# Kernel optimization log

Measured on AMD Instinct MI355X. Metric: run time of the kernel, lower is better.

The kernel has to match this reference:

```python
import jax, jax.numpy as jnp
import numpy as np

T, B, N, C, H = 4, 4, 1024, 512, 8
D = C // H
EPS = 1e-5
TAU = 2.0
SCALE = 0.125


def _bn(x, g, b, m, v):
    # eval-mode BatchNorm1d over channel dim C (last axis here)
    return (x - m) * jax.lax.rsqrt(v + EPS) * g + b


def _lif(x, v_th=1.0):
    # multi-step LIF over leading T axis: v += (x - v)/tau; spike = H(v - vth);
    # hard reset to 0 (detach_reset); sigmoid surrogate (alpha=4) straight-through
    def step(v, xt):
        v = v + (xt - v) / TAU
        sg = jax.nn.sigmoid(4.0 * (v - v_th))
        hard = (v >= v_th).astype(x.dtype)
        spike = sg + jax.lax.stop_gradient(hard - sg)
        v = v * (1.0 - jax.lax.stop_gradient(spike))
        return v, spike
    _, s = jax.lax.scan(step, jnp.zeros_like(x[0]), x)
    return s


def _heads(y):
    # [T,B,N,C] -> [T,B,H,N,D]
    return y.reshape(T, B, N, H, D).transpose(0, 1, 3, 2, 4)


def _forward(x, s_x, q_w, q_b, q_g, q_bt, q_m, q_v,
             k_w, k_b, k_g, k_bt, k_m, k_v,
             v_w, v_b, v_g, v_bt, v_m, v_v,
             p_w, p_b, p_g, p_bt, p_m, p_v):
    # s_x is flattened but never used in the original forward
    q = _heads(_lif(_bn(x @ q_w.T + q_b, q_g, q_bt, q_m, q_v)))
    k = _heads(_lif(_bn(x @ k_w.T + k_b, k_g, k_bt, k_m, k_v)))
    v = _heads(_bn(x @ v_w.T + v_b, v_g, v_bt, v_m, v_v))  # no v_lif in original forward
    attn = jnp.einsum('tbhnd,tbhmd->tbhnm', q, k) * SCALE
    o = jnp.einsum('tbhnm,tbhmd->tbhnd', attn, v)
    o = o.transpose(0, 1, 3, 2, 4).reshape(T, B, N, C)
    return _bn(o @ p_w.T + p_b, p_g, p_bt, p_m, p_v)


def setup_inputs() -> dict:
    key = jax.random.key(0)
    ks = jax.random.split(key, 10)
    def w(k):
        return jax.random.normal(k, (C, C), jnp.float32) * 0.02
    ones = jnp.ones((C,), jnp.float32)
    zeros = jnp.zeros((C,), jnp.float32)
    return {
        'x': jax.random.normal(ks[0], (T, B, N, C), jnp.float32),
        's_x': jax.random.normal(ks[1], (T, B, N, C), jnp.float32),
        'q_w': w(ks[2]), 'q_b': zeros,
        'q_g': jax.random.uniform(ks[6], (C,), jnp.float32, 0.5, 1.5), 'q_bt': zeros, 'q_m': zeros, 'q_v': ones,
        'k_w': w(ks[3]), 'k_b': zeros,
        'k_g': jax.random.uniform(ks[7], (C,), jnp.float32, 0.5, 1.5), 'k_bt': zeros, 'k_m': zeros, 'k_v': ones,
        'v_w': w(ks[4]), 'v_b': zeros,
        'v_g': jax.random.uniform(ks[8], (C,), jnp.float32, 0.5, 1.5), 'v_bt': zeros, 'v_m': zeros, 'v_v': ones,
        'p_w': w(ks[5]), 'p_b': zeros,
        'p_g': jax.random.uniform(ks[9], (C,), jnp.float32, 0.5, 1.5), 'p_bt': zeros, 'p_m': zeros, 'p_v': ones,
    }


def reference(x, s_x, q_w, q_b, q_g, q_bt, q_m, q_v,
              k_w, k_b, k_g, k_bt, k_m, k_v,
              v_w, v_b, v_g, v_bt, v_m, v_v,
              p_w, p_b, p_g, p_bt, p_m, p_v):
    return _forward(x, s_x, q_w, q_b, q_g, q_bt, q_m, q_v,
                    k_w, k_b, k_g, k_bt, k_m, k_v,
                    v_w, v_b, v_g, v_bt, v_m, v_v,
                    p_w, p_b, p_g, p_bt, p_m, p_v)
```

## Files before the change

kernel.cpp:

```cpp
#include <hip/hip_runtime.h>


#define T_ 4
#define B_ 4
#define N_ 1024
#define C_ 512
#define H_ 8
#define M_ (T_*B_*N_)

typedef __bf16 bf16x8 __attribute__((ext_vector_type(8)));
typedef float  floatx4 __attribute__((ext_vector_type(4)));

__device__ __forceinline__ float bf2f(unsigned short u) {
  union { unsigned int i; float f; } v; v.i = ((unsigned int)u) << 16; return v.f;
}
__device__ __forceinline__ unsigned short f2bf(float f) {
  unsigned int x = __float_as_uint(f);
  return (unsigned short)((x + 0x7fffu + ((x >> 16) & 1u)) >> 16);
}

#define GLOAD16(gaddr, ldsbase) \
  __builtin_amdgcn_global_load_lds((__attribute__((address_space(1))) void*)(gaddr), \
                                   (__attribute__((address_space(3))) void*)(ldsbase), 16, 0, 0)

__global__ __launch_bounds__(256) void prep_split_x(const float* __restrict__ src,
                                                    unsigned short* __restrict__ dst,
                                                    int nelem) {
  const int idx = (blockIdx.x * 256 + threadIdx.x) * 4;
  if (idx >= nelem) return;
  const float4 v = *(const float4*)(src + idx);
  const int m = idx >> 9, k = idx & 511;
  const int t = m >> 12, b = (m >> 10) & 3, n = m & 1023;
  const int mp = (((b << 10) | n) << 2) | t;
  const size_t base = (size_t)mp * 1024 + k;
  float vv[4] = {v.x, v.y, v.z, v.w};
  unsigned short h[4], l[4];
#pragma unroll
  for (int j = 0; j < 4; ++j) { h[j] = f2bf(vv[j]); l[j] = f2bf(vv[j] - bf2f(h[j])); }
  *(ushort4*)(dst + base) = ushort4{h[0], h[1], h[2], h[3]};
  *(ushort4*)(dst + base + 512) = ushort4{l[0], l[1], l[2], l[3]};
}

__global__ __launch_bounds__(256) void prep_weights(const float* __restrict__ qw,
                                                    const float* __restrict__ kw,
                                                    const float* __restrict__ vw,
                                                    const float* __restrict__ pw,
                                                    unsigned short* __restrict__ Wqk3,
                                                    unsigned short* __restrict__ Wvb,
                                                    unsigned short* __restrict__ Wpb) {
  const int z = blockIdx.z;
  const int idx = (blockIdx.x * 256 + threadIdx.x) * 4;
  if (idx >= C_ * C_) return;
  const float* src = (z == 0) ? qw : (z == 1) ? kw : (z == 2) ? vw : pw;
  const float4 v = *(const float4*)(src + idx);
  if (z >= 2) {
    unsigned short* dst = (z == 2) ? Wvb : Wpb;
    *(ushort4*)(dst + idx) = ushort4{f2bf(v.x), f2bf(v.y), f2bf(v.z), f2bf(v.w)};
    return;
  }
  const int row = idx >> 9, k = idx & 511;
  unsigned short* dst = Wqk3 + (size_t)(z * 512) * 1536;
  const size_t base = (size_t)row * 1536 + k;
  float vv[4] = {v.x, v.y, v.z, v.w};
  unsigned short h[4], l[4];
#pragma unroll
  for (int j = 0; j < 4; ++j) { h[j] = f2bf(vv[j]); l[j] = f2bf(vv[j] - bf2f(h[j])); }
  ushort4 hi{h[0], h[1], h[2], h[3]};
  *(ushort4*)(dst + base) = hi;
  *(ushort4*)(dst + base + 512) = hi;
  *(ushort4*)(dst + base + 1024) = ushort4{l[0], l[1], l[2], l[3]};
}

struct BnParams { const float* p[20]; };
__global__ __launch_bounds__(256) void bn_prep(BnParams P, float* __restrict__ scl,
                                               float* __restrict__ sft) {
  const int o = blockIdx.x * 256 + threadIdx.x;
  const int grp = o >> 9, ci = o & 511;
  const float* bias = P.p[grp * 5 + 0];
  const float* g    = P.p[grp * 5 + 1];
  const float* bt   = P.p[grp * 5 + 2];
  const float* mu   = P.p[grp * 5 + 3];
  const float* var  = P.p[grp * 5 + 4];
  const float s = g[ci] * rsqrtf(var[ci] + 1e-5f);
  scl[o] = s;
  sft[o] = (bias[ci] - mu[ci]) * s + bt[ci];
}

struct Job2 {
  const unsigned short* A; int lda;
  const unsigned short* w; int ldb;
  int K, ldc, epi;
  const float* scl; const float* sft;
  float* out32; unsigned short* out16; unsigned short* out16b;
};

__global__ __launch_bounds__(512, 2) void gemm_bn(Job2 job, int lntile) {
  const int xcd = blockIdx.x & 7, slot = blockIdx.x >> 3;
  const int ntm1 = (1 << lntile) - 1;
  const int panel = xcd + 8 * (slot >> lntile);
  const int m0 = panel * 256;
  const int n0 = (slot & ntm1) * 256;

  const int tid = threadIdx.x;
  const int wv = tid >> 6, lane = tid & 63;
  const int wm = wv >> 1, wn = wv & 1;
  const int NT = job.K >> 5;

  __shared__ unsigned short AB[4][256 * 64];

  const int rloc = lane >> 3;
  const int ulog = (lane & 7) ^ rloc;
  const bool isA = ulog < 4;
  const unsigned short* bq[4];
#pragma unroll
  for (int q = 0; q < 4; ++q) {
    const int row = wv * 32 + q * 8 + rloc;
    bq[q] = isA ? job.A + (size_t)(m0 + row) * job.lda + ulog * 8
                : job.w + (size_t)(n0 + row) * job.ldb + (ulog - 4) * 8;
  }

#define ISSUE(T_, BUF_) do {                                                 \
    const int t_ = (T_);                                                     \
    const int off_ = isA ? ((t_ < 32 ? t_ : t_ - 32) << 5) : (t_ << 5);      \
    _Pragma("unroll")                                                        \
    for (int q = 0; q < 4; ++q)                                              \
      GLOAD16(bq[q] + off_, &AB[BUF_][(wv * 32 + q * 8) * 64]);              \
  } while (0)

  const int r15 = lane & 15;
  const int apos = (lane >> 4) ^ (lane & 7);
  const int bpos = (4 | (lane >> 4)) ^ (lane & 7);
  const int aoff = (wm * 64 + r15) * 64 + apos * 8;
  const int boff = (wn * 128 + r15) * 64 + bpos * 8;

  bf16x8 A0[4], A1[4], L0[4], L1[4], Hh[4];

#define RD_ALO(BUF_, AX, LX) do {                                            \
    const unsigned short* lb_ = &AB[BUF_][0];                                \
    _Pragma("unroll")                                                        \
    for (int i_ = 0; i_ < 4; ++i_) AX[i_] = *(const bf16x8*)(lb_ + aoff + i_ * 1024); \
    _Pragma("unroll")                                                        \
    for (int j_ = 0; j_ < 4; ++j_) LX[j_] = *(const bf16x8*)(lb_ + boff + j_ * 1024); \
  } while (0)

#define RD_HI(BUF_) do {                                                     \
    const unsigned short* lb_ = &AB[BUF_][0];                                \
    _Pragma("unroll")                                                        \
    for (int j_ = 0; j_ < 4; ++j_) Hh[j_] = *(const bf16x8*)(lb_ + boff + (4 + j_) * 1024); \
  } while (0)

#define MF_LO(AX, LX) do {                                                   \
    __builtin_amdgcn_s_setprio(1);                                           \
    _Pragma("unroll")                                                        \
    for (int i_ = 0; i_ < 4; ++i_)                                           \
    _Pragma("unroll")                                                        \
      for (int j_ = 0; j_ < 4; ++j_)                                         \
        acc[i_][j_] = __builtin_amdgcn_mfma_f32_16x16x32_bf16(AX[i_], LX[j_], acc[i_][j_], 0, 0, 0); \
    __builtin_amdgcn_s_setprio(0);                                           \
  } while (0)

#define MF_HI(AX) do {                                                       \
    __builtin_amdgcn_s_setprio(1);                                           \
    _Pragma("unroll")                                                        \
    for (int i_ = 0; i_ < 4; ++i_)                                           \
    _Pragma("unroll")                                                        \
      for (int j_ = 0; j_ < 4; ++j_)                                         \
        acc[i_][4 + j_] = __builtin_amdgcn_mfma_f32_16x16x32_bf16(AX[i_], Hh[j_], acc[i_][4 + j_], 0, 0, 0); \
    __builtin_amdgcn_s_setprio(0);                                           \
  } while (0)

#define MIDBAR(N_) do {                                                      \
    asm volatile("s_waitcnt vmcnt(" #N_ ")" ::: "memory");                   \
    __builtin_amdgcn_s_barrier();                                            \
    __builtin_amdgcn_sched_barrier(0);                                       \
  } while (0)

#define SLOT_I(KT_, BC_, BN_, AX, LX, AY, LY) do {                           \
    RD_HI(BC_); MF_LO(AX, LX);                                               \
    MIDBAR(4);                                                               \
    ISSUE((KT_) + 3, (BC_ + 3) & 3);                                         \
    RD_ALO(BN_, AY, LY); MF_HI(AX);                                          \
  } while (0)

  floatx4 acc[4][8];
#pragma unroll
  for (int i = 0; i < 4; ++i)
#pragma unroll
    for (int j = 0; j < 8; ++j) acc[i][j] = floatx4{0.f, 0.f, 0.f, 0.f};

  ISSUE(0, 0); ISSUE(1, 1); ISSUE(2, 2);
  asm volatile("s_waitcnt vmcnt(4)" ::: "memory");
  __builtin_amdgcn_s_barrier();
  __builtin_amdgcn_sched_barrier(0);
  RD_ALO(0, A0, L0);

  const int NG = (NT - 4) >> 2;
  for (int g = 0; g < NG; ++g) {
    const int g4 = g << 2;
    SLOT_I(g4 + 0, 0, 1, A0, L0, A1, L1);
    SLOT_I(g4 + 1, 1, 2, A1, L1, A0, L0);
    SLOT_I(g4 + 2, 2, 3, A0, L0, A1, L1);
    SLOT_I(g4 + 3, 3, 0, A1, L1, A0, L0);
  }
  SLOT_I(NT - 4, 0, 1, A0, L0, A1, L1);
  RD_HI(1); MF_LO(A1, L1); MIDBAR(4); RD_ALO(2, A0, L0); MF_HI(A1);
  RD_HI(2); MF_LO(A0, L0); MIDBAR(0); RD_ALO(3, A1, L1); MF_HI(A0);
  RD_HI(3); MF_LO(A1, L1); MF_HI(A1);

  float scl[8], sft[8];
#pragma unroll
  for (int j = 0; j < 8; ++j) {
    const int c = n0 + wn * 128 + j * 16 + r15;
    scl[j] = job.scl[c];
    sft[j] = job.sft[c];
  }
  const int rbase = m0 + wm * 64 + (lane >> 4) * 4;

  if (job.epi == 2 && n0 < 512) {
    const int cb = n0 + wn * 128 + r15;
#pragma unroll
    for (int i = 0; i < 4; ++i) {
      unsigned short spk[4][8];
#pragma unroll
      for (int j = 0; j < 8; ++j) {
        float vme = 0.f;
#pragma unroll
        for (int r = 0; r < 4; ++r) {
          const float y = acc[i][j][r] * scl[j] + sft[j];
          vme += (y - vme) * 0.5f;
          const bool sp = vme >= 1.0f;
          spk[r][j] = sp ? (unsigned short)0x3F80 : (unsigned short)0;
          if (sp) vme = 0.f;
        }
      }
#pragma unroll
      for (int r = 0; r < 4; ++r) {
        unsigned short* prow = job.out16 + (size_t)(rbase + 16 * i + r) * 512 + cb;
#pragma unroll
        for (int j = 0; j < 8; ++j) prow[j * 16] = spk[r][j];
      }
    }
  } else if (job.epi == 2) {
    __syncthreads();
    unsigned short* lds = &AB[0][0];
    const int gq = lane >> 4;
#pragma unroll
    for (int i = 0; i < 4; ++i) {
      const int n_loc = wm * 16 + 4 * i + gq;
#pragma unroll
      for (int j = 0; j < 8; ++j) {
        const int c_loc = wn * 128 + j * 16 + r15;
        const int colbase = c_loc * 64 + (n_loc ^ ((c_loc & 7) << 3));
        float vme = 0.f;
#pragma unroll
        for (int r = 0; r < 4; ++r) {
          const float y = acc[i][j][r] * scl[j] + sft[j];
          vme += (y - vme) * 0.5f;
          const bool sp = vme >= 1.0f;
          lds[r * 16384 + colbase] = sp ? (unsigned short)0x3F80 : (unsigned short)0;
          if (sp) vme = 0.f;
        }
      }
    }
    __syncthreads();
    const int b = panel >> 4, n0g = (panel & 15) * 64, cb = n0 - 512;
#pragma unroll
    for (int it = 0; it < 16; ++it) {
      const int rho = wv * 128 + it * 8 + (lane >> 3);
      const int t = rho >> 8, c = rho & 255;
      const int nb = lane & 7;
      const uint4 d = *(const uint4*)&lds[t * 16384 + c * 64 + ((nb ^ (c & 7)) << 3)];
      *(uint4*)(job.out16b + (size_t)((t * 4 + b) * 512 + cb + c) * 1024 + n0g + nb * 8) = d;
    }
  } else {
#pragma unroll
    for (int i = 0; i < 4; ++i)
#pragma unroll
      for (int r = 0; r < 4; ++r) {
        unsigned short* prow = job.out16 + (size_t)(rbase + 16 * i + r) * job.ldc + n0 + wn * 128 + r15;
#pragma unroll
        for (int j = 0; j < 8; ++j) prow[j * 16] = f2bf(acc[i][j][r] * scl[j] + sft[j]);
      }
  }
}

__global__ __launch_bounds__(512, 2) void gemm_bn128(Job2 job) {
  const int xcd = blockIdx.x & 7, slot = blockIdx.x >> 3;
  const int panel = xcd + 8 * (slot >> 1);
  const int m0 = panel * 128;
  const int n0 = (slot & 1) * 256;

  const int tid = threadIdx.x;
  const int wv = tid >> 6, lane = tid & 63;
  const int wm = wv >> 2, wn = wv & 3;

  __shared__ unsigned short ABS[4][384 * 32];

  const unsigned short* src[3];
#pragma unroll
  for (int g = 0; g < 3; ++g) {
    const int row = wv * 48 + g * 16 + (lane >> 2);
    const int ulog = (lane & 3) ^ (row & 3);
    src[g] = (row < 128) ? job.A + (size_t)(m0 + row) * job.lda + ulog * 8
                         : job.w + (size_t)(n0 + row - 128) * job.ldb + ulog * 8;
  }

#define ISSUE1(T_, BUF_) do {                                                \
    const int k0_ = (T_) << 5;                                               \
    _Pragma("unroll")                                                        \
    for (int g_ = 0; g_ < 3; ++g_)                                           \
      GLOAD16(src[g_] + k0_, &ABS[BUF_][(wv * 48 + g_ * 16) * 32]);          \
  } while (0)

  const int r15 = lane & 15;
  const int uoff = ((lane >> 4) ^ (r15 & 3)) << 3;
  const int arow0 = (wm * 64 + r15) * 32 + uoff;
  const int brow0 = (128 + wn * 64 + r15) * 32 + uoff;

  bf16x8 AX[4], BX[4], AY[4], BY[4];
#define RD1(BUF_, A_, B_) do {                                               \
    const unsigned short* lb_ = &ABS[BUF_][0];                               \
    _Pragma("unroll")                                                        \
    for (int i_ = 0; i_ < 4; ++i_) A_[i_] = *(const bf16x8*)(lb_ + arow0 + i_ * 512); \
    _Pragma("unroll")                                                        \
    for (int j_ = 0; j_ < 4; ++j_) B_[j_] = *(const bf16x8*)(lb_ + brow0 + j_ * 512); \
  } while (0)

#define MF1(A_, B_) do {                                                     \
    __builtin_amdgcn_s_setprio(1);                                           \
    _Pragma("unroll")                                                        \
    for (int i_ = 0; i_ < 4; ++i_)                                           \
    _Pragma("unroll")                                                        \
      for (int j_ = 0; j_ < 4; ++j_)                                         \
        acc[i_][j_] = __builtin_amdgcn_mfma_f32_16x16x32_bf16(A_[i_], B_[j_], acc[i_][j_], 0, 0, 0); \
    __builtin_amdgcn_s_setprio(0);                                           \
  } while (0)

#define MB1(N_) do {                                                         \
    asm volatile("s_waitcnt vmcnt(" #N_ ")" ::: "memory");                   \
    __builtin_amdgcn_s_barrier();                                            \
    __builtin_amdgcn_sched_barrier(0);                                       \
  } while (0)

  floatx4 acc[4][4];
#pragma unroll
  for (int i = 0; i < 4; ++i)
#pragma unroll
    for (int j = 0; j < 4; ++j) acc[i][j] = floatx4{0.f, 0.f, 0.f, 0.f};

  ISSUE1(0, 0); ISSUE1(1, 1); ISSUE1(2, 2);
  asm volatile("s_waitcnt vmcnt(6)" ::: "memory");
  __builtin_amdgcn_s_barrier();
  __builtin_amdgcn_sched_barrier(0);
  RD1(0, AX, BX);

#pragma unroll 1
  for (int kt = 0; kt < 12; kt += 2) {
    MB1(3); ISSUE1(kt + 3, (kt + 3) & 3); RD1((kt + 1) & 3, AY, BY); MF1(AX, BX);
    MB1(3); ISSUE1(kt + 4, (kt + 4) & 3); RD1((kt + 2) & 3, AX, BX); MF1(AY, BY);
  }
  MB1(3); ISSUE1(15, 3); RD1(1, AY, BY); MF1(AX, BX);
  MB1(3); RD1(2, AX, BX); MF1(AY, BY);
  MB1(0); RD1(3, AY, BY); MF1(AX, BX);
  MF1(AY, BY);

  float scl[4], sft[4];
#pragma unroll
  for (int j = 0; j < 4; ++j) {
    const int c = n0 + wn * 64 + j * 16 + r15;
    scl[j] = job.scl[c];
    sft[j] = job.sft[c];
  }
  const int rbase = m0 + wm * 64 + (lane >> 4) * 4;

  if (job.epi == 4) {
    __syncthreads();
    unsigned short* lds = &ABS[0][0];
    const int gq = lane >> 4;
#pragma unroll
    for (int i = 0; i < 4; ++i) {
      const int n_loc = wm * 16 + 4 * i + gq;
#pragma unroll
      for (int j = 0; j < 4; ++j) {
        const int c_loc = wn * 64 + j * 16 + r15;
        const int colbase = c_loc * 32 + (n_loc ^ (((c_loc >> 2) & 3) << 3));
#pragma unroll
        for (int r = 0; r < 4; ++r)
          lds[r * 8192 + colbase] = f2bf(acc[i][j][r] * scl[j] + sft[j]);
      }
    }
    __syncthreads();
    const int b = panel >> 5, n0g = (panel & 31) * 32;
#pragma unroll
    for (int it = 0; it < 8; ++it) {
      const int rho = wv * 128 + it * 16 + (lane >> 2);
      const int t = rho >> 8, c = rho & 255;
      const int nb = lane & 3;
      const uint4 d = *(const uint4*)&lds[t * 8192 + c * 32 + ((nb ^ ((c >> 2) & 3)) << 3)];
      *(uint4*)(job.out16b + (size_t)((t * 4 + b) * 512 + n0 + c) * 1024 + n0g + nb * 8) = d;
    }
  } else {
#pragma unroll
    for (int i = 0; i < 4; ++i)
#pragma unroll
      for (int r = 0; r < 4; ++r) {
        const int mp = rbase + 16 * i + r;
        const int t = mp & 3, bn = mp >> 2;
        const int mstd = (((t << 2) | (bn >> 10)) << 10) | (bn & 1023);
        float* prow = job.out32 + (size_t)mstd * 512 + n0 + wn * 64 + r15;
#pragma unroll
        for (int j = 0; j < 4; ++j) prow[j * 16] = acc[i][j][r] * scl[j] + sft[j];
      }
  }
}

__global__ __launch_bounds__(256) void kv_gemm(const unsigned short* __restrict__ ktr,
                                               const unsigned short* __restrict__ vtr,
                                               float* __restrict__ kvp) {
  const int bid = blockIdx.x;
  const int head = bid >> 1;
  const int mh = bid & 1;
  const int tb = head >> 3;
  const int h = head & 7;
  const int wv = threadIdx.x >> 6, lane = threadIdx.x & 63;
  const int m0 = mh * 512 + wv * 128;
  const size_t cbase = (size_t)tb * C_ + h * 64;
  const int rsel = lane & 15, koff = (lane >> 4) * 8;

  floatx4 acc[4][4];
#pragma unroll
  for (int i = 0; i < 4; ++i)
#pragma unroll
    for (int j = 0; j < 4; ++j) acc[i][j] = floatx4{0.f, 0.f, 0.f, 0.f};

#pragma unroll
  for (int s = 0; s < 4; ++s) {
    const int m = m0 + s * 32 + koff;
    bf16x8 a[4], b[4];
#pragma unroll
    for (int dt = 0; dt < 4; ++dt)
      a[dt] = *(const bf16x8*)(ktr + (cbase + dt * 16 + rsel) * N_ + m);
#pragma unroll
    for (int et = 0; et < 4; ++et)
      b[et] = *(const bf16x8*)(vtr + (cbase + et * 16 + rsel) * N_ + m);
#pragma unroll
    for (int dt = 0; dt < 4; ++dt)
#pragma unroll
      for (int et = 0; et < 4; ++et)
        acc[dt][et] = __builtin_amdgcn_mfma_f32_16x16x32_bf16(a[dt], b[et], acc[dt][et], 0, 0, 0);
  }

  float* outp = kvp + ((size_t)head * 8 + mh * 4 + wv) * 4096;
  const int dbase = (lane >> 4) * 4;
  const int e0 = lane & 15;
#pragma unroll
  for (int dt = 0; dt < 4; ++dt)
#pragma unroll
    for (int et = 0; et < 4; ++et)
#pragma unroll
      for (int r = 0; r < 4; ++r)
        outp[(dt * 16 + dbase + r) * 64 + et * 16 + e0] = acc[dt][et][r];
}

__global__ __launch_bounds__(256) void kv_reduce(const float* __restrict__ kvp,
                                                 unsigned short* __restrict__ kvt) {
  const int gid = blockIdx.x * 256 + threadIdx.x;
  const int idx4 = gid * 4;
  const int head = idx4 >> 12;
  const int rem = idx4 & 4095;
  const int e = rem >> 6, d0 = rem & 63;
  const float* p = kvp + (size_t)head * 8 * 4096;
  unsigned short rr[4];
#pragma unroll
  for (int j = 0; j < 4; ++j) {
    float s = 0.f;
#pragma unroll
    for (int pp = 0; pp < 8; ++pp) s += p[pp * 4096 + (d0 + j) * 64 + e];
    rr[j] = f2bf(0.125f * s);
  }
  uint2 o;
  o.x = (unsigned)rr[0] | ((unsigned)rr[1] << 16);
  o.y = (unsigned)rr[2] | ((unsigned)rr[3] << 16);
  *(uint2*)(kvt + idx4) = o;
}

__global__ __launch_bounds__(256) void av_gemm(const unsigned short* __restrict__ qs,
                                               const unsigned short* __restrict__ kvt,
                                               unsigned short* __restrict__ obuf) {
  const int bx = blockIdx.x;
  const int tb = bx >> 3, nt = bx & 7;
  const int t = tb >> 2, b = tb & 3;
  const int wv = threadIdx.x >> 6, lane = threadIdx.x & 63;
  const int n0 = nt * 128 + wv * 32;
  const int rsel = lane & 15, koff = (lane >> 4) * 8;

#pragma unroll 1
  for (int h = 0; h < H_; ++h) {
    floatx4 acc[2][4];
#pragma unroll
    for (int i = 0; i < 2; ++i)
#pragma unroll
      for (int j = 0; j < 4; ++j) acc[i][j] = floatx4{0.f, 0.f, 0.f, 0.f};
    const unsigned short* kvh = kvt + ((size_t)tb * 8 + h) * 4096;
#pragma unroll
    for (int s = 0; s < 2; ++s) {
      bf16x8 a[2], bv[4];
#pragma unroll
      for (int i = 0; i < 2; ++i) {
        const int n = n0 + i * 16 + rsel;
        a[i] = *(const bf16x8*)(qs + (size_t)((((b << 10) | n) << 2) | t) * 512 + h * 64 + s * 32 + koff);
      }
#pragma unroll
      for (int et = 0; et < 4; ++et)
        bv[et] = *(const bf16x8*)(kvh + (et * 16 + rsel) * 64 + s * 32 + koff);
#pragma unroll
      for (int i = 0; i < 2; ++i)
#pragma unroll
        for (int et = 0; et < 4; ++et)
          acc[i][et] = __builtin_amdgcn_mfma_f32_16x16x32_bf16(a[i], bv[et], acc[i][et], 0, 0, 0);
    }
#pragma unroll
    for (int i = 0; i < 2; ++i)
#pragma unroll
      for (int et = 0; et < 4; ++et)
#pragma unroll
        for (int r = 0; r < 4; ++r) {
          const int n = n0 + i * 16 + (lane >> 4) * 4 + r;
          obuf[(size_t)((((b << 10) | n) << 2) | t) * 512 + h * 64 + et * 16 + rsel] = f2bf(acc[i][et][r]);
        }
  }
}

extern "C" void kernel_launch(void* const* d_in, const int* in_sizes, int n_in,
                              void* d_out, int out_size, void* d_ws, size_t ws_size,
                              hipStream_t stream) {
  const float* x  = (const float*)d_in[0];
  const float* qw = (const float*)d_in[2];
  const float* kw = (const float*)d_in[8];
  const float* vw = (const float*)d_in[14];
  const float* pw = (const float*)d_in[20];

  char* ws = (char*)d_ws;
  unsigned short* X2   = (unsigned short*)(ws + 0);
  unsigned short* Wqk3 = (unsigned short*)(ws + 33554432ull);
  unsigned short* Wvb  = (unsigned short*)(ws + 36700160ull);
  unsigned short* Wpb  = (unsigned short*)(ws + 37224448ull);
  float*          scl  = (float*)(ws + 37748736ull);
  float*          sft  = (float*)(ws + 37756928ull);
  unsigned short* qsb  = (unsigned short*)(ws + 41943040ull);
  unsigned short* ktr  = (unsigned short*)(ws + 58720256ull);
  unsigned short* vtr  = (unsigned short*)(ws + 75497472ull);
  float*          kvp  = (float*)(ws + 92274688ull);
  unsigned short* kvt  = (unsigned short*)(ws + 109051904ull);
  unsigned short* ob   = (unsigned short*)(ws + 110100480ull);

  prep_split_x<<<dim3(M_ * C_ / 4 / 256), 256, 0, stream>>>(x, X2, M_ * C_);
  prep_weights<<<dim3(C_ * C_ / 4 / 256, 1, 4), 256, 0, stream>>>(qw, kw, vw, pw, Wqk3, Wvb, Wpb);

  BnParams bp;
  bp.p[0]=(const float*)d_in[3];  bp.p[1]=(const float*)d_in[4];  bp.p[2]=(const float*)d_in[5];  bp.p[3]=(const float*)d_in[6];  bp.p[4]=(const float*)d_in[7];
  bp.p[5]=(const float*)d_in[9];  bp.p[6]=(const float*)d_in[10]; bp.p[7]=(const float*)d_in[11]; bp.p[8]=(const float*)d_in[12]; bp.p[9]=(const float*)d_in[13];
  bp.p[10]=(const float*)d_in[15];bp.p[11]=(const float*)d_in[16];bp.p[12]=(const float*)d_in[17];bp.p[13]=(const float*)d_in[18];bp.p[14]=(const float*)d_in[19];
  bp.p[15]=(const float*)d_in[21];bp.p[16]=(const float*)d_in[22];bp.p[17]=(const float*)d_in[23];bp.p[18]=(const float*)d_in[24];bp.p[19]=(const float*)d_in[25];
  bn_prep<<<dim3(8), 256, 0, stream>>>(bp, scl, sft);

  Job2 jqk{X2, 1024, Wqk3, 1536, 1536, 512, 2, scl, sft, nullptr, qsb, ktr};
  gemm_bn<<<dim3(256), 512, 0, stream>>>(jqk, 2);

  Job2 jv{X2, 1024, Wvb, 512, 512, 512, 4, scl + 1024, sft + 1024, nullptr, nullptr, vtr};
  gemm_bn128<<<dim3(256), 512, 0, stream>>>(jv);

  kv_gemm<<<dim3(256), 256, 0, stream>>>(ktr, vtr, kvp);
  kv_reduce<<<dim3(512), 256, 0, stream>>>(kvp, kvt);
  av_gemm<<<dim3(128), 256, 0, stream>>>(qsb, kvt, ob);

  Job2 jp{ob, 512, Wpb, 512, 512, 512, 3, scl + 1536, sft + 1536, (float*)d_out, nullptr, nullptr};
  gemm_bn128<<<dim3(256), 512, 0, stream>>>(jp);
}
```

Before: 141.1 us.

## Fuse prep kernels, fold KV reduction into kv_gemm via LDS, split av_gemm over heads

Merges the three preprocessing kernels (x split, weight conversion, BN folding) into one launch indexed by block id. kv_gemm now processes a whole head per block and reduces the per-wave partials in shared memory, which removes the fp32 partial buffer and the separate kv_reduce kernel. av_gemm is split across two head groups to double its grid. The goal is fewer launches and less global round-trip traffic, at the cost of halving kv_gemm's grid and adding a serialized LDS reduction with barriers.

```diff
diff --git a/kernel.cpp b/kernel.cpp
--- a/kernel.cpp
+++ b/kernel.cpp
@@ -23,67 +23,57 @@
   __builtin_amdgcn_global_load_lds((__attribute__((address_space(1))) void*)(gaddr), \
                                    (__attribute__((address_space(3))) void*)(ldsbase), 16, 0, 0)
 
-__global__ __launch_bounds__(256) void prep_split_x(const float* __restrict__ src,
-                                                    unsigned short* __restrict__ dst,
-                                                    int nelem) {
-  const int idx = (blockIdx.x * 256 + threadIdx.x) * 4;
-  if (idx >= nelem) return;
-  const float4 v = *(const float4*)(src + idx);
-  const int m = idx >> 9, k = idx & 511;
-  const int t = m >> 12, b = (m >> 10) & 3, n = m & 1023;
-  const int mp = (((b << 10) | n) << 2) | t;
-  const size_t base = (size_t)mp * 1024 + k;
-  float vv[4] = {v.x, v.y, v.z, v.w};
-  unsigned short h[4], l[4];
-#pragma unroll
-  for (int j = 0; j < 4; ++j) { h[j] = f2bf(vv[j]); l[j] = f2bf(vv[j] - bf2f(h[j])); }
-  *(ushort4*)(dst + base) = ushort4{h[0], h[1], h[2], h[3]};
-  *(ushort4*)(dst + base + 512) = ushort4{l[0], l[1], l[2], l[3]};
-}
-
-__global__ __launch_bounds__(256) void prep_weights(const float* __restrict__ qw,
-                                                    const float* __restrict__ kw,
-                                                    const float* __restrict__ vw,
-                                                    const float* __restrict__ pw,
-                                                    unsigned short* __restrict__ Wqk3,
-                                                    unsigned short* __restrict__ Wvb,
-                                                    unsigned short* __restrict__ Wpb) {
-  const int z = blockIdx.z;
-  const int idx = (blockIdx.x * 256 + threadIdx.x) * 4;
-  if (idx >= C_ * C_) return;
-  const float* src = (z == 0) ? qw : (z == 1) ? kw : (z == 2) ? vw : pw;
-  const float4 v = *(const float4*)(src + idx);
-  if (z >= 2) {
-    unsigned short* dst = (z == 2) ? Wvb : Wpb;
-    *(ushort4*)(dst + idx) = ushort4{f2bf(v.x), f2bf(v.y), f2bf(v.z), f2bf(v.w)};
-    return;
-  }
-  const int row = idx >> 9, k = idx & 511;
-  unsigned short* dst = Wqk3 + (size_t)(z * 512) * 1536;
-  const size_t base = (size_t)row * 1536 + k;
-  float vv[4] = {v.x, v.y, v.z, v.w};
-  unsigned short h[4], l[4];
-#pragma unroll
-  for (int j = 0; j < 4; ++j) { h[j] = f2bf(vv[j]); l[j] = f2bf(vv[j] - bf2f(h[j])); }
-  ushort4 hi{h[0], h[1], h[2], h[3]};
-  *(ushort4*)(dst + base) = hi;
-  *(ushort4*)(dst + base + 512) = hi;
-  *(ushort4*)(dst + base + 1024) = ushort4{l[0], l[1], l[2], l[3]};
-}
-
 struct BnParams { const float* p[20]; };
-__global__ __launch_bounds__(256) void bn_prep(BnParams P, float* __restrict__ scl,
-                                               float* __restrict__ sft) {
-  const int o = blockIdx.x * 256 + threadIdx.x;
-  const int grp = o >> 9, ci = o & 511;
-  const float* bias = P.p[grp * 5 + 0];
-  const float* g    = P.p[grp * 5 + 1];
-  const float* bt   = P.p[grp * 5 + 2];
-  const float* mu   = P.p[grp * 5 + 3];
-  const float* var  = P.p[grp * 5 + 4];
-  const float s = g[ci] * rsqrtf(var[ci] + 1e-5f);
-  scl[o] = s;
-  sft[o] = (bias[ci] - mu[ci]) * s + bt[ci];
+struct PrepArgs {
+  const float *x, *qw, *kw, *vw, *pw;
+  unsigned short *X2, *Wqk3, *Wvb, *Wpb;
+  float *scl, *sft;
+  BnParams bp;
+};
+
+__global__ __launch_bounds__(256) void prep_all(PrepArgs P) {
+  const int bid = blockIdx.x;
+  if (bid < 8192) {
+    const int idx = (bid * 256 + threadIdx.x) * 4;
+    const float4 v = *(const float4*)(P.x + idx);
+    const int m = idx >> 9, k = idx & 511;
+    const int t = m >> 12, b = (m >> 10) & 3, n = m & 1023;
+    const int mp = (((b << 10) | n) << 2) | t;
+    const size_t base = (size_t)mp * 1024 + k;
+    float vv[4] = {v.x, v.y, v.z, v.w};
+    unsigned short h[4], l[4];
+#pragma unroll
+    for (int j = 0; j < 4; ++j) { h[j] = f2bf(vv[j]); l[j] = f2bf(vv[j] - bf2f(h[j])); }
+    *(ushort4*)(P.X2 + base) = ushort4{h[0], h[1], h[2], h[3]};
+    *(ushort4*)(P.X2 + base + 512) = ushort4{l[0], l[1], l[2], l[3]};
+  } else if (bid < 9216) {
+    const int z = (bid - 8192) >> 8;
+    const int idx = ((((bid - 8192) & 255) * 256) + threadIdx.x) * 4;
+    const float* src = (z == 0) ? P.qw : (z == 1) ? P.kw : (z == 2) ? P.vw : P.pw;
+    const float4 v = *(const float4*)(src + idx);
+    if (z >= 2) {
+      unsigned short* dst = (z == 2) ? P.Wvb : P.Wpb;
+      *(ushort4*)(dst + idx) = ushort4{f2bf(v.x), f2bf(v.y), f2bf(v.z), f2bf(v.w)};
+      return;
+    }
+    const int row = idx >> 9, k = idx & 511;
+    unsigned short* dst = P.Wqk3 + (size_t)(z * 512) * 1536;
+    const size_t base = (size_t)row * 1536 + k;
+    float vv[4] = {v.x, v.y, v.z, v.w};
+    unsigned short h[4], l[4];
+#pragma unroll
+    for (int j = 0; j < 4; ++j) { h[j] = f2bf(vv[j]); l[j] = f2bf(vv[j] - bf2f(h[j])); }
+    ushort4 hi{h[0], h[1], h[2], h[3]};
+    *(ushort4*)(dst + base) = hi;
+    *(ushort4*)(dst + base + 512) = hi;
+    *(ushort4*)(dst + base + 1024) = ushort4{l[0], l[1], l[2], l[3]};
+  } else {
+    const int o = (bid - 9216) * 256 + threadIdx.x;
+    const int grp = o >> 9, ci = o & 511;
+    const float s = P.bp.p[grp * 5 + 1][ci] * rsqrtf(P.bp.p[grp * 5 + 4][ci] + 1e-5f);
+    P.scl[o] = s;
+    P.sft[o] = (P.bp.p[grp * 5 + 0][ci] - P.bp.p[grp * 5 + 3][ci]) * s + P.bp.p[grp * 5 + 2][ci];
+  }
 }
 
 struct Job2 {
@@ -416,14 +406,12 @@
 
 __global__ __launch_bounds__(256) void kv_gemm(const unsigned short* __restrict__ ktr,
                                                const unsigned short* __restrict__ vtr,
-                                               float* __restrict__ kvp) {
-  const int bid = blockIdx.x;
-  const int head = bid >> 1;
-  const int mh = bid & 1;
+                                               unsigned short* __restrict__ kvt) {
+  const int head = blockIdx.x;
   const int tb = head >> 3;
   const int h = head & 7;
   const int wv = threadIdx.x >> 6, lane = threadIdx.x & 63;
-  const int m0 = mh * 512 + wv * 128;
+  const int m0 = wv * 256;
   const size_t cbase = (size_t)tb * C_ + h * 64;
   const int rsel = lane & 15, koff = (lane >> 4) * 8;
 
@@ -434,7 +422,7 @@
     for (int j = 0; j < 4; ++j) acc[i][j] = floatx4{0.f, 0.f, 0.f, 0.f};
 
 #pragma unroll
-  for (int s = 0; s < 4; ++s) {
+  for (int s = 0; s < 8; ++s) {
     const int m = m0 + s * 32 + koff;
     bf16x8 a[4], b[4];
 #pragma unroll
@@ -450,52 +438,48 @@
         acc[dt][et] = __builtin_amdgcn_mfma_f32_16x16x32_bf16(a[dt], b[et], acc[dt][et], 0, 0, 0);
   }
 
-  float* outp = kvp + ((size_t)head * 8 + mh * 4 + wv) * 4096;
+  __shared__ float red[4096];
   const int dbase = (lane >> 4) * 4;
   const int e0 = lane & 15;
-#pragma unroll
-  for (int dt = 0; dt < 4; ++dt)
-#pragma unroll
-    for (int et = 0; et < 4; ++et)
-#pragma unroll
-      for (int r = 0; r < 4; ++r)
-        outp[(dt * 16 + dbase + r) * 64 + et * 16 + e0] = acc[dt][et][r];
-}
-
-__global__ __launch_bounds__(256) void kv_reduce(const float* __restrict__ kvp,
-                                                 unsigned short* __restrict__ kvt) {
-  const int gid = blockIdx.x * 256 + threadIdx.x;
-  const int idx4 = gid * 4;
-  const int head = idx4 >> 12;
-  const int rem = idx4 & 4095;
-  const int e = rem >> 6, d0 = rem & 63;
-  const float* p = kvp + (size_t)head * 8 * 4096;
-  unsigned short rr[4];
-#pragma unroll
-  for (int j = 0; j < 4; ++j) {
-    float s = 0.f;
-#pragma unroll
-    for (int pp = 0; pp < 8; ++pp) s += p[pp * 4096 + (d0 + j) * 64 + e];
-    rr[j] = f2bf(0.125f * s);
-  }
-  uint2 o;
-  o.x = (unsigned)rr[0] | ((unsigned)rr[1] << 16);
-  o.y = (unsigned)rr[2] | ((unsigned)rr[3] << 16);
-  *(uint2*)(kvt + idx4) = o;
+#pragma unroll 1
+  for (int w = 0; w < 4; ++w) {
+    if (wv == w) {
+#pragma unroll
+      for (int dt = 0; dt < 4; ++dt)
+#pragma unroll
+        for (int et = 0; et < 4; ++et)
+#pragma unroll
+          for (int r = 0; r < 4; ++r) {
+            const int o = (dt * 16 + dbase + r) * 64 + et * 16 + e0;
+            red[o] = (w == 0) ? acc[dt][et][r] : red[o] + acc[dt][et][r];
+          }
+    }
+    __syncthreads();
+  }
+  const int d = threadIdx.x & 63;
+  const int eg = threadIdx.x >> 6;
+#pragma unroll
+  for (int j = 0; j < 16; ++j) {
+    const int e = eg * 16 + j;
+    kvt[(size_t)head * 4096 + e * 64 + d] = f2bf(0.125f * red[d * 64 + e]);
+  }
 }
 
 __global__ __launch_bounds__(256) void av_gemm(const unsigned short* __restrict__ qs,
                                                const unsigned short* __restrict__ kvt,
                                                unsigned short* __restrict__ obuf) {
   const int bx = blockIdx.x;
-  const int tb = bx >> 3, nt = bx & 7;
+  const int tb = bx >> 4;
+  const int sub = bx & 15;
+  const int nt = sub >> 1;
+  const int h0 = (sub & 1) * 4;
   const int t = tb >> 2, b = tb & 3;
   const int wv = threadIdx.x >> 6, lane = threadIdx.x & 63;
   const int n0 = nt * 128 + wv * 32;
   const int rsel = lane & 15, koff = (lane >> 4) * 8;
 
 #pragma unroll 1
-  for (int h = 0; h < H_; ++h) {
+  for (int h = h0; h < h0 + 4; ++h) {
     floatx4 acc[2][4];
 #pragma unroll
     for (int i = 0; i < 2; ++i)
@@ -534,12 +518,6 @@
 extern "C" void kernel_launch(void* const* d_in, const int* in_sizes, int n_in,
                               void* d_out, int out_size, void* d_ws, size_t ws_size,
                               hipStream_t stream) {
-  const float* x  = (const float*)d_in[0];
-  const float* qw = (const float*)d_in[2];
-  const float* kw = (const float*)d_in[8];
-  const float* vw = (const float*)d_in[14];
-  const float* pw = (const float*)d_in[20];
-
   char* ws = (char*)d_ws;
   unsigned short* X2   = (unsigned short*)(ws + 0);
   unsigned short* Wqk3 = (unsigned short*)(ws + 33554432ull);
@@ -550,19 +528,22 @@
   unsigned short* qsb  = (unsigned short*)(ws + 41943040ull);
   unsigned short* ktr  = (unsigned short*)(ws + 58720256ull);
   unsigned short* vtr  = (unsigned short*)(ws + 75497472ull);
-  float*          kvp  = (float*)(ws + 92274688ull);
-  unsigned short* kvt  = (unsigned short*)(ws + 109051904ull);
-  unsigned short* ob   = (unsigned short*)(ws + 110100480ull);
-
-  prep_split_x<<<dim3(M_ * C_ / 4 / 256), 256, 0, stream>>>(x, X2, M_ * C_);
-  prep_weights<<<dim3(C_ * C_ / 4 / 256, 1, 4), 256, 0, stream>>>(qw, kw, vw, pw, Wqk3, Wvb, Wpb);
-
-  BnParams bp;
-  bp.p[0]=(const float*)d_in[3];  bp.p[1]=(const float*)d_in[4];  bp.p[2]=(const float*)d_in[5];  bp.p[3]=(const float*)d_in[6];  bp.p[4]=(const float*)d_in[7];
-  bp.p[5]=(const float*)d_in[9];  bp.p[6]=(const float*)d_in[10]; bp.p[7]=(const float*)d_in[11]; bp.p[8]=(const float*)d_in[12]; bp.p[9]=(const float*)d_in[13];
-  bp.p[10]=(const float*)d_in[15];bp.p[11]=(const float*)d_in[16];bp.p[12]=(const float*)d_in[17];bp.p[13]=(const float*)d_in[18];bp.p[14]=(const float*)d_in[19];
-  bp.p[15]=(const float*)d_in[21];bp.p[16]=(const float*)d_in[22];bp.p[17]=(const float*)d_in[23];bp.p[18]=(const float*)d_in[24];bp.p[19]=(const float*)d_in[25];
-  bn_prep<<<dim3(8), 256, 0, stream>>>(bp, scl, sft);
+  unsigned short* kvt  = (unsigned short*)(ws + 92274688ull);
+  unsigned short* ob   = (unsigned short*)(ws + 93323264ull);
+
+  PrepArgs pa;
+  pa.x  = (const float*)d_in[0];
+  pa.qw = (const float*)d_in[2];
+  pa.kw = (const float*)d_in[8];
+  pa.vw = (const float*)d_in[14];
+  pa.pw = (const float*)d_in[20];
+  pa.X2 = X2; pa.Wqk3 = Wqk3; pa.Wvb = Wvb; pa.Wpb = Wpb;
+  pa.scl = scl; pa.sft = sft;
+  pa.bp.p[0]=(const float*)d_in[3];  pa.bp.p[1]=(const float*)d_in[4];  pa.bp.p[2]=(const float*)d_in[5];  pa.bp.p[3]=(const float*)d_in[6];  pa.bp.p[4]=(const float*)d_in[7];
+  pa.bp.p[5]=(const float*)d_in[9];  pa.bp.p[6]=(const float*)d_in[10]; pa.bp.p[7]=(const float*)d_in[11]; pa.bp.p[8]=(const float*)d_in[12]; pa.bp.p[9]=(const float*)d_in[13];
+  pa.bp.p[10]=(const float*)d_in[15];pa.bp.p[11]=(const float*)d_in[16];pa.bp.p[12]=(const float*)d_in[17];pa.bp.p[13]=(const float*)d_in[18];pa.bp.p[14]=(const float*)d_in[19];
+  pa.bp.p[15]=(const float*)d_in[21];pa.bp.p[16]=(const float*)d_in[22];pa.bp.p[17]=(const float*)d_in[23];pa.bp.p[18]=(const float*)d_in[24];pa.bp.p[19]=(const float*)d_in[25];
+  prep_all<<<dim3(9224), 256, 0, stream>>>(pa);
 
   Job2 jqk{X2, 1024, Wqk3, 1536, 1536, 512, 2, scl, sft, nullptr, qsb, ktr};
   gemm_bn<<<dim3(256), 512, 0, stream>>>(jqk, 2);
@@ -570,9 +551,8 @@
   Job2 jv{X2, 1024, Wvb, 512, 512, 512, 4, scl + 1024, sft + 1024, nullptr, nullptr, vtr};
   gemm_bn128<<<dim3(256), 512, 0, stream>>>(jv);
 
-  kv_gemm<<<dim3(256), 256, 0, stream>>>(ktr, vtr, kvp);
-  kv_reduce<<<dim3(512), 256, 0, stream>>>(kvp, kvt);
-  av_gemm<<<dim3(128), 256, 0, stream>>>(qsb, kvt, ob);
+  kv_gemm<<<dim3(128), 256, 0, stream>>>(ktr, vtr, kvt);
+  av_gemm<<<dim3(256), 256, 0, stream>>>(qsb, kvt, ob);
 
   Job2 jp{ob, 512, Wpb, 512, 512, 512, 3, scl + 1536, sft + 1536, (float*)d_out, nullptr, nullptr};
   gemm_bn128<<<dim3(256), 512, 0, stream>>>(jp);
```

Result: faster. 126.2 us (-10.5%).
